# Kernel tuning notes

Measured on AMD Instinct MI355X. Metric: run time of the kernel, lower is better.

The kernel has to match this reference:

```python
import jax, jax.numpy as jnp
import numpy as np

N_NODES = 100000
N_EDGES = 800000
B = 4000            # number of pair subgraphs
GNN_IN = 428        # embed_dim(300) + 128 structural features
H = 64              # GIN hidden_channels
HID = 512           # PATH_DIM
EMB = 300           # numberbatch embedding dim
NUM_CLS = 151       # VG object classes
N_LAYERS = 3


def setup_inputs() -> dict:
    key = jax.random.key(0)
    ks = jax.random.split(key, 32)
    inp = {
        "pred_pairs": jax.random.randint(ks[0], (B, 2), 0, NUM_CLS, dtype=jnp.int32),
        "x": jax.random.normal(ks[1], (N_NODES, GNN_IN), dtype=jnp.float32),
        "edge_index": jax.random.randint(ks[2], (2, N_EDGES), 0, N_NODES, dtype=jnp.int32),
        "batch_ids": jnp.sort(jax.random.randint(ks[3], (N_NODES,), 0, B, dtype=jnp.int32)),
        "entity_embed": jax.random.normal(ks[4], (NUM_CLS, EMB), dtype=jnp.float32) * 0.05,
    }
    dins = [GNN_IN, H, H]
    for l in range(N_LAYERS):
        inp[f"w1_{l}"] = jax.random.normal(ks[5 + 4 * l], (dins[l], H), dtype=jnp.float32) * 0.05
        inp[f"b1_{l}"] = jnp.zeros((H,), dtype=jnp.float32)
        inp[f"w2_{l}"] = jax.random.normal(ks[6 + 4 * l], (H, H), dtype=jnp.float32) * 0.05
        inp[f"b2_{l}"] = jnp.zeros((H,), dtype=jnp.float32)
    inp["lin_w"] = jax.random.normal(ks[20], (H, HID), dtype=jnp.float32) * 0.05
    inp["lin_b"] = jnp.zeros((HID,), dtype=jnp.float32)
    inp["final_w"] = jax.random.normal(ks[21], (2 * EMB + HID, HID), dtype=jnp.float32) * 0.05
    inp["final_b"] = jnp.zeros((HID,), dtype=jnp.float32)
    return inp


def _gin_conv(h, src, dst, w1, b1, w2, b2):
    # GIN (eps=0): h_i' = MLP(h_i + sum_{j->i} h_j)
    agg = jax.ops.segment_sum(h[src], dst, num_segments=N_NODES)  # [N, d]
    z = h + agg
    z = jax.nn.relu(z @ w1 + b1)
    return jax.nn.relu(z @ w2 + b2)


def reference(pred_pairs, x, edge_index, batch_ids, entity_embed,
              w1_0, b1_0, w2_0, b2_0,
              w1_1, b1_1, w2_1, b2_1,
              w1_2, b1_2, w2_2, b2_2,
              lin_w, lin_b, final_w, final_b):
    src, dst = edge_index[0], edge_index[1]
    h = x
    for (w1, b1, w2, b2) in ((w1_0, b1_0, w2_0, b2_0),
                             (w1_1, b1_1, w2_1, b2_1),
                             (w1_2, b1_2, w2_2, b2_2)):
        h = _gin_conv(h, src, dst, w1, b1, w2, b2)
    # graph-level mean pooling over batch segments
    pooled = jax.ops.segment_sum(h, batch_ids, num_segments=B)              # [B, H]
    counts = jax.ops.segment_sum(jnp.ones((N_NODES,), h.dtype), batch_ids,
                                 num_segments=B)                            # [B]
    pooled = pooled / jnp.maximum(counts, 1.0)[:, None]
    emb = pooled @ lin_w + lin_b                                            # [B, HID]
    original = entity_embed[pred_pairs].reshape(B, 2 * EMB)                 # [B, 600]
    out = jnp.concatenate([emb, original], axis=1) @ final_w + final_b      # [B, HID]
    return out
```

## Files before the change

### kernel.cpp

```cpp
#include <hip/hip_runtime.h>
#include <hip/hip_bf16.h>

#define N_NODES 100000
#define N_EDGES 800000
#define BGRAPH  4000
#define GNN_IN  428
#define HDIM    64
#define HID     512
#define EMBD    300
#define AIN     1112
#define CAP     48
#define LSTR    72

typedef unsigned short u16;
typedef short bf16x8 __attribute__((ext_vector_type(8)));
typedef float f32x4  __attribute__((ext_vector_type(4)));

__device__ __forceinline__ u16 f2bf(float f) {
    union { float f; unsigned int u; } v; v.f = f;
    unsigned int r = v.u + 0x7FFFu + ((v.u >> 16) & 1u);
    return (u16)(r >> 16);
}
__device__ __forceinline__ float bf2f(u16 u) {
    union { unsigned int u; float f; } v; v.u = ((unsigned int)u) << 16;
    return v.f;
}

__global__ void k_prep_w0(const float* __restrict__ w, u16* __restrict__ w0T) {
    const int idx = blockIdx.x * 256 + threadIdx.x;
    if (idx >= 64 * 448) return;
    const int n = idx / 448, k = idx - n * 448;
    w0T[idx] = (k < GNN_IN) ? f2bf(w[k * 64 + n]) : (u16)0;
}
__global__ void k_prep_fw(const float* __restrict__ fw, u16* __restrict__ fwT) {
    const int idx = blockIdx.x * 256 + threadIdx.x;
    if (idx >= 512 * 1120) return;
    const int n = idx / 1120, k = idx - n * 1120;
    fwT[idx] = (k < AIN) ? f2bf(fw[(size_t)k * 512 + n]) : (u16)0;
}
__global__ void k_prep_w64(const float* __restrict__ w, u16* __restrict__ wT) {
    const int idx = blockIdx.x * 256 + threadIdx.x;
    const int k = idx >> 6, o = idx & 63;
    wT[o * 64 + k] = f2bf(w[idx]);
}

__global__ __launch_bounds__(256) void k_gemm_xw(const float* __restrict__ x,
                                                 const u16* __restrict__ w0T,
                                                 u16* __restrict__ y) {
    const int t = threadIdx.x;
    const int lane = t & 63, wave = t >> 6;
    const int q = lane >> 4, m = lane & 15;
    const int n0 = blockIdx.x * 64;
    const int row = min(n0 + wave * 16 + m, N_NODES - 1);
    const float* __restrict__ xr = &x[(size_t)row * GNN_IN];

    f32x4 acc[4];
#pragma unroll
    for (int c = 0; c < 4; ++c) acc[c] = (f32x4){0.f, 0.f, 0.f, 0.f};

    for (int k0 = 0; k0 < 448; k0 += 32) {
        const int ka = k0 + q * 8;
        float4 va = {0.f, 0.f, 0.f, 0.f}, vb = {0.f, 0.f, 0.f, 0.f};
        if (ka + 4 <= GNN_IN) va = *reinterpret_cast<const float4*>(xr + ka);
        if (ka + 8 <= GNN_IN) vb = *reinterpret_cast<const float4*>(xr + ka + 4);
        bf16x8 a;
        a[0] = (short)f2bf(va.x); a[1] = (short)f2bf(va.y);
        a[2] = (short)f2bf(va.z); a[3] = (short)f2bf(va.w);
        a[4] = (short)f2bf(vb.x); a[5] = (short)f2bf(vb.y);
        a[6] = (short)f2bf(vb.z); a[7] = (short)f2bf(vb.w);
#pragma unroll
        for (int c = 0; c < 4; ++c) {
            const bf16x8 b = *reinterpret_cast<const bf16x8*>(&w0T[(c * 16 + m) * 448 + ka]);
            acc[c] = __builtin_amdgcn_mfma_f32_16x16x32_bf16(a, b, acc[c], 0, 0, 0);
        }
    }
#pragma unroll
    for (int c = 0; c < 4; ++c)
#pragma unroll
        for (int r = 0; r < 4; ++r) {
            const int rr = n0 + wave * 16 + q * 4 + r;
            if (rr < N_NODES) y[(size_t)rr * 64 + c * 16 + m] = f2bf(acc[c][r]);
        }
}

__global__ void k_fill(const int* __restrict__ ei, int* __restrict__ deg,
                       int* __restrict__ csr2) {
    const int e = blockIdx.x * blockDim.x + threadIdx.x;
    if (e >= N_EDGES) return;
    const int s = ei[e];
    const int d = ei[N_EDGES + e];
    const int slot = atomicAdd(&deg[d], 1);
    if (slot < CAP) csr2[d * CAP + slot] = s;
}

__global__ void k_counts(const int* __restrict__ bids, float* __restrict__ counts) {
    const int n = blockIdx.x * blockDim.x + threadIdx.x;
    if (n >= N_NODES) return;
    atomicAdd(&counts[bids[n]], 1.0f);
}

__device__ __forceinline__ float gather16p(const u16* __restrict__ hin,
                                           const int* __restrict__ lst,
                                           int dg, int lane, float u) {
    const int4* l4 = reinterpret_cast<const int4*>(lst);
    const int4 ia = l4[0], ib = l4[1], ic = l4[2], id4 = l4[3];
    int id[16] = {ia.x, ia.y, ia.z, ia.w, ib.x, ib.y, ib.z, ib.w,
                  ic.x, ic.y, ic.z, ic.w, id4.x, id4.y, id4.z, id4.w};
    float v[16];
#pragma unroll
    for (int i = 0; i < 16; ++i) {
        const bool ok = (i < dg);
        const int idx = ok ? id[i] : 0;
        v[i] = bf2f(hin[(size_t)idx * 64 + lane]) * (ok ? 1.f : 0.f);
    }
#pragma unroll
    for (int i = 0; i < 16; ++i) u += v[i];
    if (__builtin_expect(dg > 16, 0)) {
        for (int e = 16; e < dg; e += 8) {
            const int4 a = l4[e >> 2];
            const int4 b = l4[(e >> 2) + 1];
            int id2[8] = {a.x, a.y, a.z, a.w, b.x, b.y, b.z, b.w};
#pragma unroll
            for (int i = 0; i < 8; ++i) {
                const bool ok = (e + i < dg);
                const int idx = ok ? id2[i] : 0;
                u += bf2f(hin[(size_t)idx * 64 + lane]) * (ok ? 1.f : 0.f);
            }
        }
    }
    return u;
}

__global__ __launch_bounds__(256, 4) void k_gin0(const u16* __restrict__ y,
                                                 const int* __restrict__ deg,
                                                 const int* __restrict__ csr2,
                                                 const float* __restrict__ b1,
                                                 const u16* __restrict__ w2T,
                                                 const float* __restrict__ b2,
                                                 u16* __restrict__ hout) {
    __shared__ u16 zs[64 * LSTR];
    const int t = threadIdx.x;
    const int lane = t & 63, wave = t >> 6;
    const int q = lane >> 4, m = lane & 15;
    const int n0 = blockIdx.x * 64;
    const int base = n0 + wave * 16;
    const float b1v = b1[lane];
#pragma unroll 2
    for (int j = 0; j < 16; ++j) {
        const int n = min(base + j, N_NODES - 1);
        const int dg = min(deg[n], CAP);
        float u = bf2f(y[(size_t)n * 64 + lane]);
        u = gather16p(y, &csr2[n * CAP], dg, lane, u);
        zs[(wave * 16 + j) * LSTR + lane] = f2bf(fmaxf(u + b1v, 0.f));
    }
    f32x4 acc[4];
#pragma unroll
    for (int c = 0; c < 4; ++c) acc[c] = (f32x4){0.f, 0.f, 0.f, 0.f};
    const bf16x8 a0 = *reinterpret_cast<const bf16x8*>(&zs[(wave * 16 + m) * LSTR + q * 8]);
    const bf16x8 a1 = *reinterpret_cast<const bf16x8*>(&zs[(wave * 16 + m) * LSTR + 32 + q * 8]);
#pragma unroll
    for (int c = 0; c < 4; ++c) {
        const bf16x8 bb0 = *reinterpret_cast<const bf16x8*>(&w2T[(c * 16 + m) * 64 + q * 8]);
        const bf16x8 bb1 = *reinterpret_cast<const bf16x8*>(&w2T[(c * 16 + m) * 64 + 32 + q * 8]);
        acc[c] = __builtin_amdgcn_mfma_f32_16x16x32_bf16(a0, bb0, acc[c], 0, 0, 0);
        acc[c] = __builtin_amdgcn_mfma_f32_16x16x32_bf16(a1, bb1, acc[c], 0, 0, 0);
    }
#pragma unroll
    for (int c = 0; c < 4; ++c) {
        const float bb = b2[c * 16 + m];
#pragma unroll
        for (int r = 0; r < 4; ++r) {
            const int n = n0 + wave * 16 + q * 4 + r;
            if (n < N_NODES) hout[(size_t)n * 64 + c * 16 + m] = f2bf(fmaxf(acc[c][r] + bb, 0.f));
        }
    }
}

__device__ __forceinline__ void gin_mfma2(const u16* __restrict__ hin,
                                          const int* __restrict__ deg,
                                          const int* __restrict__ csr2,
                                          const u16* __restrict__ w1T,
                                          const float* __restrict__ b1,
                                          const u16* __restrict__ w2T,
                                          u16* us, u16* zs,
                                          int n0, int t, f32x4 acc[4]) {
    const int lane = t & 63, wave = t >> 6;
    const int q = lane >> 4, m = lane & 15;
    const int base = n0 + wave * 16;
#pragma unroll 2
    for (int j = 0; j < 16; ++j) {
        const int n = min(base + j, N_NODES - 1);
        const int dg = min(deg[n], CAP);
        float u = bf2f(hin[(size_t)n * 64 + lane]);
        u = gather16p(hin, &csr2[n * CAP], dg, lane, u);
        us[(wave * 16 + j) * LSTR + lane] = f2bf(u);
    }
    f32x4 z[4];
#pragma unroll
    for (int c = 0; c < 4; ++c) z[c] = (f32x4){0.f, 0.f, 0.f, 0.f};
    {
        const bf16x8 a0 = *reinterpret_cast<const bf16x8*>(&us[(wave * 16 + m) * LSTR + q * 8]);
        const bf16x8 a1 = *reinterpret_cast<const bf16x8*>(&us[(wave * 16 + m) * LSTR + 32 + q * 8]);
#pragma unroll
        for (int c = 0; c < 4; ++c) {
            const bf16x8 bb0 = *reinterpret_cast<const bf16x8*>(&w1T[(c * 16 + m) * 64 + q * 8]);
            const bf16x8 bb1 = *reinterpret_cast<const bf16x8*>(&w1T[(c * 16 + m) * 64 + 32 + q * 8]);
            z[c] = __builtin_amdgcn_mfma_f32_16x16x32_bf16(a0, bb0, z[c], 0, 0, 0);
            z[c] = __builtin_amdgcn_mfma_f32_16x16x32_bf16(a1, bb1, z[c], 0, 0, 0);
        }
    }
#pragma unroll
    for (int c = 0; c < 4; ++c) {
        const float bb = b1[c * 16 + m];
#pragma unroll
        for (int r = 0; r < 4; ++r)
            zs[(wave * 16 + q * 4 + r) * LSTR + c * 16 + m] = f2bf(fmaxf(z[c][r] + bb, 0.f));
    }
#pragma unroll
    for (int c = 0; c < 4; ++c) acc[c] = (f32x4){0.f, 0.f, 0.f, 0.f};
    {
        const bf16x8 a0 = *reinterpret_cast<const bf16x8*>(&zs[(wave * 16 + m) * LSTR + q * 8]);
        const bf16x8 a1 = *reinterpret_cast<const bf16x8*>(&zs[(wave * 16 + m) * LSTR + 32 + q * 8]);
#pragma unroll
        for (int c = 0; c < 4; ++c) {
            const bf16x8 bb0 = *reinterpret_cast<const bf16x8*>(&w2T[(c * 16 + m) * 64 + q * 8]);
            const bf16x8 bb1 = *reinterpret_cast<const bf16x8*>(&w2T[(c * 16 + m) * 64 + 32 + q * 8]);
            acc[c] = __builtin_amdgcn_mfma_f32_16x16x32_bf16(a0, bb0, acc[c], 0, 0, 0);
            acc[c] = __builtin_amdgcn_mfma_f32_16x16x32_bf16(a1, bb1, acc[c], 0, 0, 0);
        }
    }
}

__global__ __launch_bounds__(256, 4) void k_gin(const u16* __restrict__ hin,
                                                const int* __restrict__ deg,
                                                const int* __restrict__ csr2,
                                                const u16* __restrict__ w1T,
                                                const float* __restrict__ b1,
                                                const u16* __restrict__ w2T,
                                                const float* __restrict__ b2,
                                                u16* __restrict__ hout) {
    __shared__ u16 us[64 * LSTR];
    __shared__ u16 zs[64 * LSTR];
    const int t = threadIdx.x;
    const int lane = t & 63, wave = t >> 6;
    const int q = lane >> 4, m = lane & 15;
    const int n0 = blockIdx.x * 64;
    f32x4 acc[4];
    gin_mfma2(hin, deg, csr2, w1T, b1, w2T, us, zs, n0, t, acc);
#pragma unroll
    for (int c = 0; c < 4; ++c) {
        const float bb = b2[c * 16 + m];
#pragma unroll
        for (int r = 0; r < 4; ++r) {
            const int n = n0 + wave * 16 + q * 4 + r;
            if (n < N_NODES) hout[(size_t)n * 64 + c * 16 + m] = f2bf(fmaxf(acc[c][r] + bb, 0.f));
        }
    }
}

__global__ __launch_bounds__(256, 4) void k_gin_pool(const u16* __restrict__ hin,
                                                     const int* __restrict__ deg,
                                                     const int* __restrict__ csr2,
                                                     const u16* __restrict__ w1T,
                                                     const float* __restrict__ b1,
                                                     const u16* __restrict__ w2T,
                                                     const float* __restrict__ b2,
                                                     const int* __restrict__ bids,
                                                     float* __restrict__ pooled) {
    __shared__ u16 us[64 * LSTR];
    __shared__ u16 zs[64 * LSTR];
    const int t = threadIdx.x;
    const int lane = t & 63, wave = t >> 6;
    const int q = lane >> 4, m = lane & 15;
    const int n0 = blockIdx.x * 64;
    f32x4 acc[4];
    gin_mfma2(hin, deg, csr2, w1T, b1, w2T, us, zs, n0, t, acc);
#pragma unroll
    for (int c = 0; c < 4; ++c) {
        const float bb = b2[c * 16 + m];
#pragma unroll
        for (int r = 0; r < 4; ++r)
            us[(wave * 16 + q * 4 + r) * LSTR + c * 16 + m] = f2bf(fmaxf(acc[c][r] + bb, 0.f));
    }
    const int base = n0 + wave * 16;
    if (base < N_NODES) {
        float s = 0.f;
        int cur = bids[base];
        for (int j = 0; j < 16; ++j) {
            const int n = base + j;
            if (n >= N_NODES) break;
            const int b = bids[n];
            const float h = bf2f(us[(wave * 16 + j) * LSTR + lane]);
            if (b != cur) {
                atomicAdd(&pooled[cur * 64 + lane], s);
                cur = b; s = h;
            } else {
                s += h;
            }
        }
        atomicAdd(&pooled[cur * 64 + lane], s);
    }
}

__global__ __launch_bounds__(256) void k_emb(const float* __restrict__ pooled,
                                             const float* __restrict__ counts,
                                             const float* __restrict__ lw,
                                             const float* __restrict__ lb,
                                             u16* __restrict__ A) {
    __shared__ float prow[8][64];
    const int b0 = blockIdx.x * 8;
    const int t = threadIdx.x;
    const int lane = t & 63, wave = t >> 6;
    for (int i = 0; i < 2; ++i) {
        const int r = i * 4 + wave;
        const int b = b0 + r;
        const float c = fmaxf(counts[b], 1.0f);
        prow[r][lane] = pooled[b * 64 + lane] / c;
    }
    __syncthreads();
    for (int o = t; o < 512; o += 256) {
        float acc[8];
#pragma unroll
        for (int r = 0; r < 8; ++r) acc[r] = lb[o];
        for (int k = 0; k < 64; ++k) {
            const float wv = lw[k * 512 + o];
#pragma unroll
            for (int r = 0; r < 8; ++r) acc[r] += prow[r][k] * wv;
        }
#pragma unroll
        for (int r = 0; r < 8; ++r) A[(size_t)(b0 + r) * AIN + o] = f2bf(acc[r]);
    }
}

__global__ void k_orig(const int* __restrict__ pp, const float* __restrict__ ee,
                       u16* __restrict__ A) {
    const int idx = blockIdx.x * blockDim.x + threadIdx.x;
    if (idx >= BGRAPH * 600) return;
    const int b = idx / 600;
    const int j = idx - b * 600;
    const int which = (j >= 300) ? 1 : 0;
    const int cls = pp[b * 2 + which];
    A[(size_t)b * AIN + 512 + j] = f2bf(ee[cls * 300 + (j - which * 300)]);
}

__global__ __launch_bounds__(256) void k_final(const u16* __restrict__ A,
                                               const u16* __restrict__ fwT,
                                               const float* __restrict__ fb,
                                               float* __restrict__ out) {
    __shared__ u16 as[64 * 40];
    const int t = threadIdx.x;
    const int lane = t & 63, wave = t >> 6;
    const int q = lane >> 4, m = lane & 15;
    const int r0 = blockIdx.x * 64, c0 = blockIdx.y * 64;

    f32x4 acc[4];
#pragma unroll
    for (int c = 0; c < 4; ++c) acc[c] = (f32x4){0.f, 0.f, 0.f, 0.f};

    const int row = t >> 2, seg = t & 3;
    for (int k0 = 0; k0 < 1120; k0 += 32) {
        const int gr = r0 + row, gk = k0 + seg * 8;
        uint4 v = {0u, 0u, 0u, 0u};
        if (gr < BGRAPH && gk < AIN)
            v = *reinterpret_cast<const uint4*>(&A[(size_t)gr * AIN + gk]);
        *reinterpret_cast<uint4*>(&as[row * 40 + seg * 8]) = v;
        __syncthreads();
        const bf16x8 a = *reinterpret_cast<const bf16x8*>(&as[(wave * 16 + m) * 40 + q * 8]);
#pragma unroll
        for (int c = 0; c < 4; ++c) {
            const bf16x8 b = *reinterpret_cast<const bf16x8*>(&fwT[(size_t)(c0 + c * 16 + m) * 1120 + k0 + q * 8]);
            acc[c] = __builtin_amdgcn_mfma_f32_16x16x32_bf16(a, b, acc[c], 0, 0, 0);
        }
        __syncthreads();
    }
#pragma unroll
    for (int c = 0; c < 4; ++c) {
        const float bb = fb[c0 + c * 16 + m];
#pragma unroll
        for (int r = 0; r < 4; ++r) {
            const int rr = r0 + wave * 16 + q * 4 + r;
            if (rr < BGRAPH) out[(size_t)rr * 512 + c0 + c * 16 + m] = acc[c][r] + bb;
        }
    }
}

extern "C" void kernel_launch(void* const* d_in, const int* in_sizes, int n_in,
                              void* d_out, int out_size, void* d_ws, size_t ws_size,
                              hipStream_t stream) {
    const int*   pred_pairs = (const int*)d_in[0];
    const float* x          = (const float*)d_in[1];
    const int*   ei         = (const int*)d_in[2];
    const int*   bids       = (const int*)d_in[3];
    const float* ee         = (const float*)d_in[4];
    const float* w1_0 = (const float*)d_in[5];
    const float* b1_0 = (const float*)d_in[6];
    const float* w2_0 = (const float*)d_in[7];
    const float* b2_0 = (const float*)d_in[8];
    const float* w1_1 = (const float*)d_in[9];
    const float* b1_1 = (const float*)d_in[10];
    const float* w2_1 = (const float*)d_in[11];
    const float* b2_1 = (const float*)d_in[12];
    const float* w1_2 = (const float*)d_in[13];
    const float* b1_2 = (const float*)d_in[14];
    const float* w2_2 = (const float*)d_in[15];
    const float* b2_2 = (const float*)d_in[16];
    const float* lin_w   = (const float*)d_in[17];
    const float* lin_b   = (const float*)d_in[18];
    const float* final_w = (const float*)d_in[19];
    const float* final_b = (const float*)d_in[20];
    float* out = (float*)d_out;

    u16*   Y      = (u16*)d_ws;
    u16*   Hb     = Y + (size_t)N_NODES * 64;
    int*   csr2   = (int*)(Hb + (size_t)N_NODES * 64);
    int*   deg    = csr2 + (size_t)N_NODES * CAP;
    float* pooled = (float*)(deg + N_NODES);
    float* counts = pooled + (size_t)BGRAPH * 64;
    u16*   A      = (u16*)(counts + BGRAPH);
    u16*   w0T    = A + (size_t)BGRAPH * AIN;
    u16*   fwT    = w0T + 64 * 448;
    u16*   w2T0   = fwT + (size_t)512 * 1120;
    u16*   w1T1   = w2T0 + 4096;
    u16*   w2T1   = w1T1 + 4096;
    u16*   w1T2   = w2T1 + 4096;
    u16*   w2T2   = w1T2 + 4096;

    hipMemsetAsync(deg, 0, (size_t)(N_NODES + BGRAPH * 64 + BGRAPH) * sizeof(int), stream);

    k_prep_w0<<<(64 * 448 + 255) / 256, 256, 0, stream>>>(w1_0, w0T);
    k_prep_fw<<<(512 * 1120 + 255) / 256, 256, 0, stream>>>(final_w, fwT);
    k_prep_w64<<<16, 256, 0, stream>>>(w2_0, w2T0);
    k_prep_w64<<<16, 256, 0, stream>>>(w1_1, w1T1);
    k_prep_w64<<<16, 256, 0, stream>>>(w2_1, w2T1);
    k_prep_w64<<<16, 256, 0, stream>>>(w1_2, w1T2);
    k_prep_w64<<<16, 256, 0, stream>>>(w2_2, w2T2);
    k_fill<<<(N_EDGES + 255) / 256, 256, 0, stream>>>(ei, deg, csr2);
    k_counts<<<(N_NODES + 255) / 256, 256, 0, stream>>>(bids, counts);
    k_gemm_xw<<<(N_NODES + 63) / 64, 256, 0, stream>>>(x, w0T, Y);
    k_gin0<<<(N_NODES + 63) / 64, 256, 0, stream>>>(Y, deg, csr2, b1_0, w2T0, b2_0, Hb);
    k_gin<<<(N_NODES + 63) / 64, 256, 0, stream>>>(Hb, deg, csr2, w1T1, b1_1, w2T1, b2_1, Y);
    k_gin_pool<<<(N_NODES + 63) / 64, 256, 0, stream>>>(Y, deg, csr2, w1T2, b1_2, w2T2, b2_2, bids, pooled);
    k_emb<<<BGRAPH / 8, 256, 0, stream>>>(pooled, counts, lin_w, lin_b, A);
    k_orig<<<(BGRAPH * 600 + 255) / 256, 256, 0, stream>>>(pred_pairs, ee, A);
    k_final<<<dim3((BGRAPH + 63) / 64, 8), 256, 0, stream>>>(A, fwT, final_b, out);
}
```

Baseline: 603.1 us.

## Split GIN layers into per-node aggregation and separate MLP kernels

Each GIN layer's fused gather+MLP kernel is split into a one-node-per-wave aggregation kernel (k_agg) and a separate MFMA MLP kernel that reads the aggregated rows from a new workspace buffer U. The goal is to raise occupancy and memory-level parallelism in the irregular gather, at the cost of an extra global round trip of the 100k x 64 bf16 activations per layer. The final GEMM now uses a padded A stride and reads A directly from global memory without LDS staging or barriers. The five small weight-transpose launches are merged into one kernel.

```diff
diff --git a/kernel.cpp b/kernel.cpp
--- a/kernel.cpp
+++ b/kernel.cpp
@@ -9,6 +9,7 @@
 #define HID     512
 #define EMBD    300
 #define AIN     1112
+#define ASTR    1120
 #define CAP     48
 #define LSTR    72
 
@@ -38,10 +39,15 @@
     const int n = idx / 1120, k = idx - n * 1120;
     fwT[idx] = (k < AIN) ? f2bf(fw[(size_t)k * 512 + n]) : (u16)0;
 }
-__global__ void k_prep_w64(const float* __restrict__ w, u16* __restrict__ wT) {
+__global__ void k_prep_w5(const float* __restrict__ wa, const float* __restrict__ wb,
+                          const float* __restrict__ wc, const float* __restrict__ wd,
+                          const float* __restrict__ we, u16* __restrict__ wT5) {
     const int idx = blockIdx.x * 256 + threadIdx.x;
-    const int k = idx >> 6, o = idx & 63;
-    wT[o * 64 + k] = f2bf(w[idx]);
+    const int seg = idx >> 12, within = idx & 4095;
+    const int k = within >> 6, o = within & 63;
+    const float* src = (seg == 0) ? wa : (seg == 1) ? wb : (seg == 2) ? wc
+                     : (seg == 3) ? wd : we;
+    wT5[seg * 4096 + o * 64 + k] = f2bf(src[within]);
 }
 
 __global__ __launch_bounds__(256) void k_gemm_xw(const float* __restrict__ x,
@@ -99,41 +105,120 @@
     atomicAdd(&counts[bids[n]], 1.0f);
 }
 
-__device__ __forceinline__ float gather16p(const u16* __restrict__ hin,
-                                           const int* __restrict__ lst,
-                                           int dg, int lane, float u) {
-    const int4* l4 = reinterpret_cast<const int4*>(lst);
-    const int4 ia = l4[0], ib = l4[1], ic = l4[2], id4 = l4[3];
-    int id[16] = {ia.x, ia.y, ia.z, ia.w, ib.x, ib.y, ib.z, ib.w,
-                  ic.x, ic.y, ic.z, ic.w, id4.x, id4.y, id4.z, id4.w};
-    float v[16];
-#pragma unroll
-    for (int i = 0; i < 16; ++i) {
+template <int BIASRELU>
+__global__ __launch_bounds__(256, 8) void k_agg(const u16* __restrict__ hin,
+                                                const int* __restrict__ deg,
+                                                const int* __restrict__ csr2,
+                                                const float* __restrict__ b1,
+                                                u16* __restrict__ uout) {
+    const int wave = threadIdx.x >> 6, lane = threadIdx.x & 63;
+    const int n = blockIdx.x * 4 + wave;
+    if (n >= N_NODES) return;
+    const int dg = min(deg[n], CAP);
+    const int4* l4 = reinterpret_cast<const int4*>(&csr2[(size_t)n * CAP]);
+    const int4 i0 = l4[0], i1 = l4[1];
+    const int id[8] = {i0.x, i0.y, i0.z, i0.w, i1.x, i1.y, i1.z, i1.w};
+    float u = bf2f(hin[(size_t)n * 64 + lane]);
+    float v[8];
+#pragma unroll
+    for (int i = 0; i < 8; ++i) {
         const bool ok = (i < dg);
-        const int idx = ok ? id[i] : 0;
-        v[i] = bf2f(hin[(size_t)idx * 64 + lane]) * (ok ? 1.f : 0.f);
-    }
-#pragma unroll
-    for (int i = 0; i < 16; ++i) u += v[i];
-    if (__builtin_expect(dg > 16, 0)) {
-        for (int e = 16; e < dg; e += 8) {
-            const int4 a = l4[e >> 2];
-            const int4 b = l4[(e >> 2) + 1];
-            int id2[8] = {a.x, a.y, a.z, a.w, b.x, b.y, b.z, b.w};
+        const int ix = ok ? id[i] : 0;
+        v[i] = ok ? bf2f(hin[(size_t)ix * 64 + lane]) : 0.f;
+    }
+#pragma unroll
+    for (int i = 0; i < 8; ++i) u += v[i];
+    if (__builtin_expect(dg > 8, 0)) {
+        for (int e = 8; e < dg; e += 8) {
+            const int4 a4 = l4[e >> 2];
+            const int4 b4 = l4[(e >> 2) + 1];
+            const int jd[8] = {a4.x, a4.y, a4.z, a4.w, b4.x, b4.y, b4.z, b4.w};
 #pragma unroll
             for (int i = 0; i < 8; ++i) {
                 const bool ok = (e + i < dg);
-                const int idx = ok ? id2[i] : 0;
-                u += bf2f(hin[(size_t)idx * 64 + lane]) * (ok ? 1.f : 0.f);
+                const int ix = ok ? jd[i] : 0;
+                u += ok ? bf2f(hin[(size_t)ix * 64 + lane]) : 0.f;
             }
         }
     }
-    return u;
-}
-
-__global__ __launch_bounds__(256, 4) void k_gin0(const u16* __restrict__ y,
-                                                 const int* __restrict__ deg,
-                                                 const int* __restrict__ csr2,
+    if (BIASRELU) u = fmaxf(u + b1[lane], 0.f);
+    uout[(size_t)n * 64 + lane] = f2bf(u);
+}
+
+__global__ __launch_bounds__(256, 4) void k_mlp1(const u16* __restrict__ z,
+                                                 const u16* __restrict__ w2T,
+                                                 const float* __restrict__ b2,
+                                                 u16* __restrict__ hout) {
+    const int t = threadIdx.x;
+    const int lane = t & 63, wave = t >> 6;
+    const int q = lane >> 4, m = lane & 15;
+    const int base = blockIdx.x * 64 + wave * 16;
+    const int rowm = min(base + m, N_NODES - 1);
+    const bf16x8 a0 = *reinterpret_cast<const bf16x8*>(&z[(size_t)rowm * 64 + q * 8]);
+    const bf16x8 a1 = *reinterpret_cast<const bf16x8*>(&z[(size_t)rowm * 64 + 32 + q * 8]);
+    f32x4 acc[4];
+#pragma unroll
+    for (int c = 0; c < 4; ++c) acc[c] = (f32x4){0.f, 0.f, 0.f, 0.f};
+#pragma unroll
+    for (int c = 0; c < 4; ++c) {
+        const bf16x8 bb0 = *reinterpret_cast<const bf16x8*>(&w2T[(c * 16 + m) * 64 + q * 8]);
+        const bf16x8 bb1 = *reinterpret_cast<const bf16x8*>(&w2T[(c * 16 + m) * 64 + 32 + q * 8]);
+        acc[c] = __builtin_amdgcn_mfma_f32_16x16x32_bf16(a0, bb0, acc[c], 0, 0, 0);
+        acc[c] = __builtin_amdgcn_mfma_f32_16x16x32_bf16(a1, bb1, acc[c], 0, 0, 0);
+    }
+#pragma unroll
+    for (int c = 0; c < 4; ++c) {
+        const float bb = b2[c * 16 + m];
+#pragma unroll
+        for (int r = 0; r < 4; ++r) {
+            const int n = base + q * 4 + r;
+            if (n < N_NODES) hout[(size_t)n * 64 + c * 16 + m] = f2bf(fmaxf(acc[c][r] + bb, 0.f));
+        }
+    }
+}
+
+__device__ __forceinline__ void mlp2_core(const u16* __restrict__ u,
+                                          const u16* __restrict__ w1T,
+                                          const float* __restrict__ b1,
+                                          const u16* __restrict__ w2T,
+                                          u16* zs, int base, int t, f32x4 acc[4]) {
+    const int lane = t & 63, wave = t >> 6;
+    const int q = lane >> 4, m = lane & 15;
+    const int rowm = min(base + m, N_NODES - 1);
+    const bf16x8 a0 = *reinterpret_cast<const bf16x8*>(&u[(size_t)rowm * 64 + q * 8]);
+    const bf16x8 a1 = *reinterpret_cast<const bf16x8*>(&u[(size_t)rowm * 64 + 32 + q * 8]);
+    f32x4 z[4];
+#pragma unroll
+    for (int c = 0; c < 4; ++c) z[c] = (f32x4){0.f, 0.f, 0.f, 0.f};
+#pragma unroll
+    for (int c = 0; c < 4; ++c) {
+        const bf16x8 bb0 = *reinterpret_cast<const bf16x8*>(&w1T[(c * 16 + m) * 64 + q * 8]);
+        const bf16x8 bb1 = *reinterpret_cast<const bf16x8*>(&w1T[(c * 16 + m) * 64 + 32 + q * 8]);
+        z[c] = __builtin_amdgcn_mfma_f32_16x16x32_bf16(a0, bb0, z[c], 0, 0, 0);
+        z[c] = __builtin_amdgcn_mfma_f32_16x16x32_bf16(a1, bb1, z[c], 0, 0, 0);
+    }
+#pragma unroll
+    for (int c = 0; c < 4; ++c) {
+        const float bb = b1[c * 16 + m];
+#pragma unroll
+        for (int r = 0; r < 4; ++r)
+            zs[(wave * 16 + q * 4 + r) * LSTR + c * 16 + m] = f2bf(fmaxf(z[c][r] + bb, 0.f));
+    }
+    const bf16x8 c0v = *reinterpret_cast<const bf16x8*>(&zs[(wave * 16 + m) * LSTR + q * 8]);
+    const bf16x8 c1v = *reinterpret_cast<const bf16x8*>(&zs[(wave * 16 + m) * LSTR + 32 + q * 8]);
+#pragma unroll
+    for (int c = 0; c < 4; ++c) acc[c] = (f32x4){0.f, 0.f, 0.f, 0.f};
+#pragma unroll
+    for (int c = 0; c < 4; ++c) {
+        const bf16x8 bb0 = *reinterpret_cast<const bf16x8*>(&w2T[(c * 16 + m) * 64 + q * 8]);
+        const bf16x8 bb1 = *reinterpret_cast<const bf16x8*>(&w2T[(c * 16 + m) * 64 + 32 + q * 8]);
+        acc[c] = __builtin_amdgcn_mfma_f32_16x16x32_bf16(c0v, bb0, acc[c], 0, 0, 0);
+        acc[c] = __builtin_amdgcn_mfma_f32_16x16x32_bf16(c1v, bb1, acc[c], 0, 0, 0);
+    }
+}
+
+__global__ __launch_bounds__(256, 4) void k_mlp2(const u16* __restrict__ u,
+                                                 const u16* __restrict__ w1T,
                                                  const float* __restrict__ b1,
                                                  const u16* __restrict__ w2T,
                                                  const float* __restrict__ b2,
@@ -142,147 +227,41 @@
     const int t = threadIdx.x;
     const int lane = t & 63, wave = t >> 6;
     const int q = lane >> 4, m = lane & 15;
-    const int n0 = blockIdx.x * 64;
-    const int base = n0 + wave * 16;
-    const float b1v = b1[lane];
-#pragma unroll 2
-    for (int j = 0; j < 16; ++j) {
-        const int n = min(base + j, N_NODES - 1);
-        const int dg = min(deg[n], CAP);
-        float u = bf2f(y[(size_t)n * 64 + lane]);
-        u = gather16p(y, &csr2[n * CAP], dg, lane, u);
-        zs[(wave * 16 + j) * LSTR + lane] = f2bf(fmaxf(u + b1v, 0.f));
-    }
+    const int base = blockIdx.x * 64 + wave * 16;
     f32x4 acc[4];
-#pragma unroll
-    for (int c = 0; c < 4; ++c) acc[c] = (f32x4){0.f, 0.f, 0.f, 0.f};
-    const bf16x8 a0 = *reinterpret_cast<const bf16x8*>(&zs[(wave * 16 + m) * LSTR + q * 8]);
-    const bf16x8 a1 = *reinterpret_cast<const bf16x8*>(&zs[(wave * 16 + m) * LSTR + 32 + q * 8]);
-#pragma unroll
-    for (int c = 0; c < 4; ++c) {
-        const bf16x8 bb0 = *reinterpret_cast<const bf16x8*>(&w2T[(c * 16 + m) * 64 + q * 8]);
-        const bf16x8 bb1 = *reinterpret_cast<const bf16x8*>(&w2T[(c * 16 + m) * 64 + 32 + q * 8]);
-        acc[c] = __builtin_amdgcn_mfma_f32_16x16x32_bf16(a0, bb0, acc[c], 0, 0, 0);
-        acc[c] = __builtin_amdgcn_mfma_f32_16x16x32_bf16(a1, bb1, acc[c], 0, 0, 0);
-    }
+    mlp2_core(u, w1T, b1, w2T, zs, base, t, acc);
 #pragma unroll
     for (int c = 0; c < 4; ++c) {
         const float bb = b2[c * 16 + m];
 #pragma unroll
         for (int r = 0; r < 4; ++r) {
-            const int n = n0 + wave * 16 + q * 4 + r;
+            const int n = base + q * 4 + r;
             if (n < N_NODES) hout[(size_t)n * 64 + c * 16 + m] = f2bf(fmaxf(acc[c][r] + bb, 0.f));
         }
     }
 }
 
-__device__ __forceinline__ void gin_mfma2(const u16* __restrict__ hin,
-                                          const int* __restrict__ deg,
-                                          const int* __restrict__ csr2,
-                                          const u16* __restrict__ w1T,
-                                          const float* __restrict__ b1,
-                                          const u16* __restrict__ w2T,
-                                          u16* us, u16* zs,
-                                          int n0, int t, f32x4 acc[4]) {
-    const int lane = t & 63, wave = t >> 6;
-    const int q = lane >> 4, m = lane & 15;
-    const int base = n0 + wave * 16;
-#pragma unroll 2
-    for (int j = 0; j < 16; ++j) {
-        const int n = min(base + j, N_NODES - 1);
-        const int dg = min(deg[n], CAP);
-        float u = bf2f(hin[(size_t)n * 64 + lane]);
-        u = gather16p(hin, &csr2[n * CAP], dg, lane, u);
-        us[(wave * 16 + j) * LSTR + lane] = f2bf(u);
-    }
-    f32x4 z[4];
-#pragma unroll
-    for (int c = 0; c < 4; ++c) z[c] = (f32x4){0.f, 0.f, 0.f, 0.f};
-    {
-        const bf16x8 a0 = *reinterpret_cast<const bf16x8*>(&us[(wave * 16 + m) * LSTR + q * 8]);
-        const bf16x8 a1 = *reinterpret_cast<const bf16x8*>(&us[(wave * 16 + m) * LSTR + 32 + q * 8]);
-#pragma unroll
-        for (int c = 0; c < 4; ++c) {
-            const bf16x8 bb0 = *reinterpret_cast<const bf16x8*>(&w1T[(c * 16 + m) * 64 + q * 8]);
-            const bf16x8 bb1 = *reinterpret_cast<const bf16x8*>(&w1T[(c * 16 + m) * 64 + 32 + q * 8]);
-            z[c] = __builtin_amdgcn_mfma_f32_16x16x32_bf16(a0, bb0, z[c], 0, 0, 0);
-            z[c] = __builtin_amdgcn_mfma_f32_16x16x32_bf16(a1, bb1, z[c], 0, 0, 0);
-        }
-    }
-#pragma unroll
-    for (int c = 0; c < 4; ++c) {
-        const float bb = b1[c * 16 + m];
+__global__ __launch_bounds__(256, 4) void k_mlp2_pool(const u16* __restrict__ u,
+                                                      const u16* __restrict__ w1T,
+                                                      const float* __restrict__ b1,
+                                                      const u16* __restrict__ w2T,
+                                                      const float* __restrict__ b2,
+                                                      const int* __restrict__ bids,
+                                                      float* __restrict__ pooled) {
+    __shared__ u16 zs[64 * LSTR];
+    const int t = threadIdx.x;
+    const int lane = t & 63, wave = t >> 6;
+    const int q = lane >> 4, m = lane & 15;
+    const int base = blockIdx.x * 64 + wave * 16;
+    f32x4 acc[4];
+    mlp2_core(u, w1T, b1, w2T, zs, base, t, acc);
+#pragma unroll
+    for (int c = 0; c < 4; ++c) {
+        const float bb = b2[c * 16 + m];
 #pragma unroll
         for (int r = 0; r < 4; ++r)
-            zs[(wave * 16 + q * 4 + r) * LSTR + c * 16 + m] = f2bf(fmaxf(z[c][r] + bb, 0.f));
-    }
-#pragma unroll
-    for (int c = 0; c < 4; ++c) acc[c] = (f32x4){0.f, 0.f, 0.f, 0.f};
-    {
-        const bf16x8 a0 = *reinterpret_cast<const bf16x8*>(&zs[(wave * 16 + m) * LSTR + q * 8]);
-        const bf16x8 a1 = *reinterpret_cast<const bf16x8*>(&zs[(wave * 16 + m) * LSTR + 32 + q * 8]);
-#pragma unroll
-        for (int c = 0; c < 4; ++c) {
-            const bf16x8 bb0 = *reinterpret_cast<const bf16x8*>(&w2T[(c * 16 + m) * 64 + q * 8]);
-            const bf16x8 bb1 = *reinterpret_cast<const bf16x8*>(&w2T[(c * 16 + m) * 64 + 32 + q * 8]);
-            acc[c] = __builtin_amdgcn_mfma_f32_16x16x32_bf16(a0, bb0, acc[c], 0, 0, 0);
-            acc[c] = __builtin_amdgcn_mfma_f32_16x16x32_bf16(a1, bb1, acc[c], 0, 0, 0);
-        }
-    }
-}
-
-__global__ __launch_bounds__(256, 4) void k_gin(const u16* __restrict__ hin,
-                                                const int* __restrict__ deg,
-                                                const int* __restrict__ csr2,
-                                                const u16* __restrict__ w1T,
-                                                const float* __restrict__ b1,
-                                                const u16* __restrict__ w2T,
-                                                const float* __restrict__ b2,
-                                                u16* __restrict__ hout) {
-    __shared__ u16 us[64 * LSTR];
-    __shared__ u16 zs[64 * LSTR];
-    const int t = threadIdx.x;
-    const int lane = t & 63, wave = t >> 6;
-    const int q = lane >> 4, m = lane & 15;
-    const int n0 = blockIdx.x * 64;
-    f32x4 acc[4];
-    gin_mfma2(hin, deg, csr2, w1T, b1, w2T, us, zs, n0, t, acc);
-#pragma unroll
-    for (int c = 0; c < 4; ++c) {
-        const float bb = b2[c * 16 + m];
-#pragma unroll
-        for (int r = 0; r < 4; ++r) {
-            const int n = n0 + wave * 16 + q * 4 + r;
-            if (n < N_NODES) hout[(size_t)n * 64 + c * 16 + m] = f2bf(fmaxf(acc[c][r] + bb, 0.f));
-        }
-    }
-}
-
-__global__ __launch_bounds__(256, 4) void k_gin_pool(const u16* __restrict__ hin,
-                                                     const int* __restrict__ deg,
-                                                     const int* __restrict__ csr2,
-                                                     const u16* __restrict__ w1T,
-                                                     const float* __restrict__ b1,
-                                                     const u16* __restrict__ w2T,
-                                                     const float* __restrict__ b2,
-                                                     const int* __restrict__ bids,
-                                                     float* __restrict__ pooled) {
-    __shared__ u16 us[64 * LSTR];
-    __shared__ u16 zs[64 * LSTR];
-    const int t = threadIdx.x;
-    const int lane = t & 63, wave = t >> 6;
-    const int q = lane >> 4, m = lane & 15;
-    const int n0 = blockIdx.x * 64;
-    f32x4 acc[4];
-    gin_mfma2(hin, deg, csr2, w1T, b1, w2T, us, zs, n0, t, acc);
-#pragma unroll
-    for (int c = 0; c < 4; ++c) {
-        const float bb = b2[c * 16 + m];
-#pragma unroll
-        for (int r = 0; r < 4; ++r)
-            us[(wave * 16 + q * 4 + r) * LSTR + c * 16 + m] = f2bf(fmaxf(acc[c][r] + bb, 0.f));
-    }
-    const int base = n0 + wave * 16;
+            zs[(wave * 16 + q * 4 + r) * LSTR + c * 16 + m] = f2bf(fmaxf(acc[c][r] + bb, 0.f));
+    }
     if (base < N_NODES) {
         float s = 0.f;
         int cur = bids[base];
@@ -290,7 +269,7 @@
             const int n = base + j;
             if (n >= N_NODES) break;
             const int b = bids[n];
-            const float h = bf2f(us[(wave * 16 + j) * LSTR + lane]);
+            const float h = bf2f(zs[(wave * 16 + j) * LSTR + lane]);
             if (b != cur) {
                 atomicAdd(&pooled[cur * 64 + lane], s);
                 cur = b; s = h;
@@ -328,57 +307,55 @@
             for (int r = 0; r < 8; ++r) acc[r] += prow[r][k] * wv;
         }
 #pragma unroll
-        for (int r = 0; r < 8; ++r) A[(size_t)(b0 + r) * AIN + o] = f2bf(acc[r]);
+        for (int r = 0; r < 8; ++r) A[(size_t)(b0 + r) * ASTR + o] = f2bf(acc[r]);
     }
 }
 
 __global__ void k_orig(const int* __restrict__ pp, const float* __restrict__ ee,
                        u16* __restrict__ A) {
     const int idx = blockIdx.x * blockDim.x + threadIdx.x;
-    if (idx >= BGRAPH * 600) return;
-    const int b = idx / 600;
-    const int j = idx - b * 600;
-    const int which = (j >= 300) ? 1 : 0;
-    const int cls = pp[b * 2 + which];
-    A[(size_t)b * AIN + 512 + j] = f2bf(ee[cls * 300 + (j - which * 300)]);
-}
-
-__global__ __launch_bounds__(256) void k_final(const u16* __restrict__ A,
-                                               const u16* __restrict__ fwT,
-                                               const float* __restrict__ fb,
-                                               float* __restrict__ out) {
-    __shared__ u16 as[64 * 40];
-    const int t = threadIdx.x;
-    const int lane = t & 63, wave = t >> 6;
-    const int q = lane >> 4, m = lane & 15;
-    const int r0 = blockIdx.x * 64, c0 = blockIdx.y * 64;
+    if (idx >= BGRAPH * 608) return;
+    const int b = idx / 608;
+    const int j = idx - b * 608;
+    u16 v = 0;
+    if (j < 600) {
+        const int which = (j >= 300) ? 1 : 0;
+        const int cls = pp[b * 2 + which];
+        v = f2bf(ee[cls * 300 + (j - which * 300)]);
+    }
+    A[(size_t)b * ASTR + 512 + j] = v;
+}
+
+__global__ __launch_bounds__(256, 4) void k_final(const u16* __restrict__ A,
+                                                  const u16* __restrict__ fwT,
+                                                  const float* __restrict__ fb,
+                                                  float* __restrict__ out) {
+    const int t = threadIdx.x;
+    const int lane = t & 63, wave = t >> 6;
+    const int q = lane >> 4, m = lane & 15;
+    const int base = blockIdx.x * 64 + wave * 16;
+    const int c0 = blockIdx.y * 64;
+    const int rowm = min(base + m, BGRAPH - 1);
+    const u16* __restrict__ ar = &A[(size_t)rowm * ASTR];
 
     f32x4 acc[4];
 #pragma unroll
     for (int c = 0; c < 4; ++c) acc[c] = (f32x4){0.f, 0.f, 0.f, 0.f};
-
-    const int row = t >> 2, seg = t & 3;
+#pragma unroll 5
     for (int k0 = 0; k0 < 1120; k0 += 32) {
-        const int gr = r0 + row, gk = k0 + seg * 8;
-        uint4 v = {0u, 0u, 0u, 0u};
-        if (gr < BGRAPH && gk < AIN)
-            v = *reinterpret_cast<const uint4*>(&A[(size_t)gr * AIN + gk]);
-        *reinterpret_cast<uint4*>(&as[row * 40 + seg * 8]) = v;
-        __syncthreads();
-        const bf16x8 a = *reinterpret_cast<const bf16x8*>(&as[(wave * 16 + m) * 40 + q * 8]);
+        const bf16x8 a = *reinterpret_cast<const bf16x8*>(&ar[k0 + q * 8]);
 #pragma unroll
         for (int c = 0; c < 4; ++c) {
             const bf16x8 b = *reinterpret_cast<const bf16x8*>(&fwT[(size_t)(c0 + c * 16 + m) * 1120 + k0 + q * 8]);
             acc[c] = __builtin_amdgcn_mfma_f32_16x16x32_bf16(a, b, acc[c], 0, 0, 0);
         }
-        __syncthreads();
     }
 #pragma unroll
     for (int c = 0; c < 4; ++c) {
         const float bb = fb[c0 + c * 16 + m];
 #pragma unroll
         for (int r = 0; r < 4; ++r) {
-            const int rr = r0 + wave * 16 + q * 4 + r;
+            const int rr = base + q * 4 + r;
             if (rr < BGRAPH) out[(size_t)rr * 512 + c0 + c * 16 + m] = acc[c][r] + bb;
         }
     }
@@ -412,35 +389,36 @@
 
     u16*   Y      = (u16*)d_ws;
     u16*   Hb     = Y + (size_t)N_NODES * 64;
-    int*   csr2   = (int*)(Hb + (size_t)N_NODES * 64);
+    u16*   U      = Hb + (size_t)N_NODES * 64;
+    int*   csr2   = (int*)(U + (size_t)N_NODES * 64);
     int*   deg    = csr2 + (size_t)N_NODES * CAP;
     float* pooled = (float*)(deg + N_NODES);
     float* counts = pooled + (size_t)BGRAPH * 64;
     u16*   A      = (u16*)(counts + BGRAPH);
-    u16*   w0T    = A + (size_t)BGRAPH * AIN;
+    u16*   w0T    = A + (size_t)BGRAPH * ASTR;
     u16*   fwT    = w0T + 64 * 448;
-    u16*   w2T0   = fwT + (size_t)512 * 1120;
-    u16*   w1T1   = w2T0 + 4096;
-    u16*   w2T1   = w1T1 + 4096;
-    u16*   w1T2   = w2T1 + 4096;
-    u16*   w2T2   = w1T2 + 4096;
+    u16*   wT5    = fwT + (size_t)512 * 1120;
+    u16*   w2T0   = wT5;
+    u16*   w1T1   = wT5 + 4096;
+    u16*   w2T1   = wT5 + 8192;
+    u16*   w1T2   = wT5 + 12288;
+    u16*   w2T2   = wT5 + 16384;
 
     hipMemsetAsync(deg, 0, (size_t)(N_NODES + BGRAPH * 64 + BGRAPH) * sizeof(int), stream);
 
     k_prep_w0<<<(64 * 448 + 255) / 256, 256, 0, stream>>>(w1_0, w0T);
     k_prep_fw<<<(512 * 1120 + 255) / 256, 256, 0, stream>>>(final_w, fwT);
-    k_prep_w64<<<16, 256, 0, stream>>>(w2_0, w2T0);
-    k_prep_w64<<<16, 256, 0, stream>>>(w1_1, w1T1);
-    k_prep_w64<<<16, 256, 0, stream>>>(w2_1, w2T1);
-    k_prep_w64<<<16, 256, 0, stream>>>(w1_2, w1T2);
-    k_prep_w64<<<16, 256, 0, stream>>>(w2_2, w2T2);
+    k_prep_w5<<<80, 256, 0, stream>>>(w2_0, w1_1, w2_1, w1_2, w2_2, wT5);
     k_fill<<<(N_EDGES + 255) / 256, 256, 0, stream>>>(ei, deg, csr2);
     k_counts<<<(N_NODES + 255) / 256, 256, 0, stream>>>(bids, counts);
     k_gemm_xw<<<(N_NODES + 63) / 64, 256, 0, stream>>>(x, w0T, Y);
-    k_gin0<<<(N_NODES + 63) / 64, 256, 0, stream>>>(Y, deg, csr2, b1_0, w2T0, b2_0, Hb);
-    k_gin<<<(N_NODES + 63) / 64, 256, 0, stream>>>(Hb, deg, csr2, w1T1, b1_1, w2T1, b2_1, Y);
-    k_gin_pool<<<(N_NODES + 63) / 64, 256, 0, stream>>>(Y, deg, csr2, w1T2, b1_2, w2T2, b2_2, bids, pooled);
+    k_agg<1><<<(N_NODES + 3) / 4, 256, 0, stream>>>(Y, deg, csr2, b1_0, U);
+    k_mlp1<<<(N_NODES + 63) / 64, 256, 0, stream>>>(U, w2T0, b2_0, Hb);
+    k_agg<0><<<(N_NODES + 3) / 4, 256, 0, stream>>>(Hb, deg, csr2, b1_0, U);
+    k_mlp2<<<(N_NODES + 63) / 64, 256, 0, stream>>>(U, w1T1, b1_1, w2T1, b2_1, Y);
+    k_agg<0><<<(N_NODES + 3) / 4, 256, 0, stream>>>(Y, deg, csr2, b1_0, U);
+    k_mlp2_pool<<<(N_NODES + 63) / 64, 256, 0, stream>>>(U, w1T2, b1_2, w2T2, b2_2, bids, pooled);
     k_emb<<<BGRAPH / 8, 256, 0, stream>>>(pooled, counts, lin_w, lin_b, A);
-    k_orig<<<(BGRAPH * 600 + 255) / 256, 256, 0, stream>>>(pred_pairs, ee, A);
+    k_orig<<<(BGRAPH * 608 + 255) / 256, 256, 0, stream>>>(pred_pairs, ee, A);
     k_final<<<dim3((BGRAPH + 63) / 64, 8), 256, 0, stream>>>(A, fwT, final_b, out);
 }
```

After: 676.8 us. 12.2% more time.
